# Performance work log

Measured on AMD Instinct MI355X. Metric: run time of the kernel, lower is better.

The kernel has to match this reference:

```python
import jax, jax.numpy as jnp
import numpy as np

EPS = 1e-5
DN = ('NCHW', 'OIHW', 'NCHW')


def ternarize(w):
    """Ternary Weight Network quantization with straight-through estimator.
    delta = 0.7 * mean|w|; alpha = mean of |w| over kept entries.
    """
    aw = jnp.abs(w)
    delta = 0.7 * aw.mean()
    mask = (aw > delta).astype(w.dtype)
    alpha = (aw * mask).sum() / jnp.maximum(mask.sum(), 1.0)
    q = alpha * jnp.sign(w) * mask
    return w + jax.lax.stop_gradient(q - w)


def bn(y, g, b, m, v):
    scale = (g / jnp.sqrt(v + EPS))[None, :, None, None]
    shift = (b - m * g / jnp.sqrt(v + EPS))[None, :, None, None]
    return y * scale + shift


def relu6(y):
    return jnp.clip(y, 0.0, 6.0)


def conv(x, w, stride=1, padding='VALID'):
    return jax.lax.conv_general_dilated(
        x, w, window_strides=(stride, stride), padding=padding,
        dimension_numbers=DN)


def setup_inputs() -> dict:
    key = jax.random.key(0)
    ks = jax.random.split(key, 16)
    inp, oup, expand = 32, 32, 6
    hidden = inp * expand  # 192
    B, H, W = 16, 112, 112
    d = {}
    d['x'] = jax.random.normal(ks[0], (B, inp, H, W), dtype=jnp.float32)
    # 1x1 expand conv
    d['w1'] = jax.random.normal(ks[1], (hidden, inp, 1, 1), dtype=jnp.float32) * 0.1
    d['g1'] = 1.0 + 0.1 * jax.random.normal(ks[2], (hidden,), dtype=jnp.float32)
    d['b1'] = 0.1 * jax.random.normal(ks[3], (hidden,), dtype=jnp.float32)
    d['m1'] = 0.1 * jax.random.normal(ks[4], (hidden,), dtype=jnp.float32)
    d['v1'] = jax.random.uniform(ks[5], (hidden,), minval=0.5, maxval=1.5, dtype=jnp.float32)
    # 3x3 dense conv (no groups in the source -> dense, not depthwise)
    d['w2'] = jax.random.normal(ks[6], (hidden, hidden, 3, 3), dtype=jnp.float32) * 0.05
    d['g2'] = 1.0 + 0.1 * jax.random.normal(ks[7], (hidden,), dtype=jnp.float32)
    d['b2'] = 0.1 * jax.random.normal(ks[8], (hidden,), dtype=jnp.float32)
    d['m2'] = 0.1 * jax.random.normal(ks[9], (hidden,), dtype=jnp.float32)
    d['v2'] = jax.random.uniform(ks[10], (hidden,), minval=0.5, maxval=1.5, dtype=jnp.float32)
    # 1x1 project conv
    d['w3'] = jax.random.normal(ks[11], (oup, hidden, 1, 1), dtype=jnp.float32) * 0.1
    d['g3'] = 1.0 + 0.1 * jax.random.normal(ks[12], (oup,), dtype=jnp.float32)
    d['b3'] = 0.1 * jax.random.normal(ks[13], (oup,), dtype=jnp.float32)
    d['m3'] = 0.1 * jax.random.normal(ks[14], (oup,), dtype=jnp.float32)
    d['v3'] = jax.random.uniform(ks[15], (oup,), minval=0.5, maxval=1.5, dtype=jnp.float32)
    return d


def reference(x, w1, g1, b1, m1, v1, w2, g2, b2, m2, v2, w3, g3, b3, m3, v3):
    # expand: 1x1 ternary conv -> BN -> ReLU6
    h = relu6(bn(conv(x, ternarize(w1)), g1, b1, m1, v1))
    # 3x3 ternary conv (stride=1, padding=1) -> BN -> ReLU6
    h = relu6(bn(conv(h, ternarize(w2), stride=1, padding=((1, 1), (1, 1))), g2, b2, m2, v2))
    # project: 1x1 ternary conv -> BN (no activation)
    h = bn(conv(h, ternarize(w3)), g3, b3, m3, v3)
    # residual connection (stride==1 and inp==oup)
    return x + h
```

## Files before the change

### kernel.cpp

```cpp
#include <hip/hip_runtime.h>


typedef __bf16 bf16x8 __attribute__((ext_vector_type(8)));
typedef __bf16 bf16x4 __attribute__((ext_vector_type(4)));
typedef float  f32x4  __attribute__((ext_vector_type(4)));

#define EPSBN 1e-5f

__device__ __forceinline__ void glds16(const void* g, void* l) {
  __builtin_amdgcn_global_load_lds(
      (const __attribute__((address_space(1))) void*)g,
      (__attribute__((address_space(3))) void*)l, 16, 0, 0);
}

__device__ __forceinline__ __bf16 tern(float w, float delta) {
  float aw = fabsf(w);
  float q = (aw > delta) ? ((w > 0.0f) ? 1.0f : -1.0f) : 0.0f;
  return (__bf16)q;
}


__global__ void stats_pass1(const float* __restrict__ w1, const float* __restrict__ w2,
                            const float* __restrict__ w3, double* __restrict__ pa) {
  __shared__ double red[256];
  int b = blockIdx.x, tid = threadIdx.x;
  int tix = b >> 5, slice = b & 31;
  const float* w = (tix == 0) ? w1 : (tix == 1) ? w2 : w3;
  int len = (tix == 1) ? 331776 : 6144;
  int per = len >> 5;
  int start = slice * per, end = start + per;
  double s = 0.0;
  for (int i = start + tid; i < end; i += 256) s += (double)fabsf(w[i]);
  red[tid] = s; __syncthreads();
  for (int off = 128; off > 0; off >>= 1) {
    if (tid < off) red[tid] += red[tid + off];
    __syncthreads();
  }
  if (tid == 0) pa[b] = red[0];
}

__global__ void stats_pass2(const float* __restrict__ w1, const float* __restrict__ w2,
                            const float* __restrict__ w3, const double* __restrict__ pa,
                            double* __restrict__ ps2, double* __restrict__ pc2) {
  __shared__ double red[256];
  int b = blockIdx.x, tid = threadIdx.x;
  int tix = b >> 5, slice = b & 31;
  const float* w = (tix == 0) ? w1 : (tix == 1) ? w2 : w3;
  int len = (tix == 1) ? 331776 : 6144;
  double tot = 0.0;
  for (int k = 0; k < 32; ++k) tot += pa[tix * 32 + k];
  float delta = 0.7f * (float)(tot / (double)len);
  int per = len >> 5;
  int start = slice * per, end = start + per;
  double s2 = 0.0, c2 = 0.0;
  for (int i = start + tid; i < end; i += 256) {
    float aw = fabsf(w[i]);
    if (aw > delta) { s2 += (double)aw; c2 += 1.0; }
  }
  red[tid] = s2; __syncthreads();
  for (int off = 128; off > 0; off >>= 1) {
    if (tid < off) red[tid] += red[tid + off];
    __syncthreads();
  }
  if (tid == 0) ps2[b] = red[0];
  __syncthreads();
  red[tid] = c2; __syncthreads();
  for (int off = 128; off > 0; off >>= 1) {
    if (tid < off) red[tid] += red[tid + off];
    __syncthreads();
  }
  if (tid == 0) pc2[b] = red[0];
}

__global__ void pack_kernel(
    const float* __restrict__ w1, const float* __restrict__ w2, const float* __restrict__ w3,
    const float* __restrict__ g1, const float* __restrict__ b1, const float* __restrict__ m1, const float* __restrict__ v1,
    const float* __restrict__ g2, const float* __restrict__ b2, const float* __restrict__ m2, const float* __restrict__ v2,
    const float* __restrict__ g3, const float* __restrict__ b3, const float* __restrict__ m3, const float* __restrict__ v3,
    const double* __restrict__ pa, const double* __restrict__ ps2, const double* __restrict__ pc2,
    __bf16* __restrict__ w1p, __bf16* __restrict__ w2p, __bf16* __restrict__ w3p,
    float* __restrict__ sc1, float* __restrict__ sh1,
    float* __restrict__ sc2, float* __restrict__ sh2,
    float* __restrict__ sc3, float* __restrict__ sh3) {
  __shared__ float sst[6];
  int tid = threadIdx.x;
  if (tid < 3) {
    double tot = 0.0, s2 = 0.0, c2 = 0.0;
    for (int k = 0; k < 32; ++k) {
      tot += pa[tid * 32 + k];
      s2  += ps2[tid * 32 + k];
      c2  += pc2[tid * 32 + k];
    }
    int len = (tid == 1) ? 331776 : 6144;
    sst[tid * 2]     = 0.7f * (float)(tot / (double)len);
    sst[tid * 2 + 1] = (float)(s2 / fmax(c2, 1.0));
  }
  __syncthreads();

  int idx = blockIdx.x * 256 + tid;
  if (idx < 331776) {
    float delta2 = sst[2];
    int c = idx / 6144, rem = idx - c * 6144;
    int co = rem >> 5, r5 = rem & 31;
    int cp = r5 >> 3, lo = r5 & 7;
    int tap = c / 6, cb = c - tap * 6;
    int ci = ((cp ^ ((co >> 2) & 3)) << 3) | lo;
    int cifull = cb * 32 + ci;
    w2p[idx] = tern(w2[(co * 192 + cifull) * 9 + tap], delta2);
    return;
  }
  idx -= 331776;
  if (idx < 6144) {
    int co = idx >> 5, c = (idx >> 3) & 3, lo = idx & 7;
    int ci = ((c ^ ((co >> 2) & 3)) << 3) | lo;
    w1p[idx] = tern(w1[co * 32 + ci], sst[0]);
    return;
  }
  idx -= 6144;
  if (idx < 6144) {
    int kc = idx >> 11, rem = idx & 2047;
    int co = rem >> 6, c = (rem >> 3) & 7, lo = rem & 7;
    int ci = ((c ^ (co & 7)) << 3) | lo;
    w3p[idx] = tern(w3[co * 192 + kc * 64 + ci], sst[4]);
    return;
  }
  idx -= 6144;
  if (idx < 192) {
    float rs = rsqrtf(v1[idx] + EPSBN);
    sc1[idx] = g1[idx] * rs * sst[1];
    sh1[idx] = b1[idx] - m1[idx] * g1[idx] * rs;
    return;
  }
  idx -= 192;
  if (idx < 192) {
    float rs = rsqrtf(v2[idx] + EPSBN);
    sc2[idx] = g2[idx] * rs * sst[3];
    sh2[idx] = b2[idx] - m2[idx] * g2[idx] * rs;
    return;
  }
  idx -= 192;
  if (idx < 32) {
    float rs = rsqrtf(v3[idx] + EPSBN);
    sc3[idx] = g3[idx] * rs * sst[5];
    sh3[idx] = b3[idx] - m3[idx] * g3[idx] * rs;
  }
}

__global__ __launch_bounds__(256)
void conv1_kernel(const float* __restrict__ x, const __bf16* __restrict__ w1p,
                  const float* __restrict__ scale1, const float* __restrict__ shift1,
                  __bf16* __restrict__ h1p) {
  __shared__ __align__(16) char smem[57344];
  char* smA = smem;
  char* smB = smem + 7168;
  char* Pb  = smem;
  int tid = threadIdx.x, lane = tid & 63, wave = tid >> 6;
  int h = blockIdx.x, n = blockIdx.y;

  for (int t = wave; t < 12; t += 4)
    glds16((const char*)w1p + t * 1024 + lane * 16, smB + t * 1024);

  const float* xrow = x + (long)n * 401408 + h * 112;
#pragma unroll
  for (int i = 0; i < 4; ++i) {
    int g = i * 256 + tid;
    if (g < 896) {
      int ci0 = (g / 112) * 4, w = g - (g / 112) * 112;
      const float* p = xrow + ci0 * 12544 + w;
      bf16x4 v;
      v[0] = (__bf16)p[0];
      v[1] = (__bf16)p[12544];
      v[2] = (__bf16)p[25088];
      v[3] = (__bf16)p[37632];
      int col = ((ci0 >> 3) ^ ((w >> 2) & 3));
      *(bf16x4*)(smA + w * 64 + (col << 4) + (ci0 & 7) * 2) = v;
    }
  }
  __syncthreads();

  int mrow = lane & 15, quad = lane >> 4;
  int col16 = (quad ^ ((mrow >> 2) & 3)) * 16;
  int c0 = wave * 48;

  bf16x8 aw[3], bv[7];
#pragma unroll
  for (int ic = 0; ic < 3; ++ic)
    aw[ic] = *(const bf16x8*)(smB + (c0 + ic * 16 + mrow) * 64 + col16);
#pragma unroll
  for (int jp = 0; jp < 7; ++jp)
    bv[jp] = *(const bf16x8*)(smA + (jp * 16 + mrow) * 64 + col16);

  asm volatile("s_waitcnt lgkmcnt(0)" ::: "memory");
  __builtin_amdgcn_s_barrier();
  __builtin_amdgcn_sched_barrier(0);

  f32x4 acc[7][3];
#pragma unroll
  for (int jp = 0; jp < 7; ++jp)
#pragma unroll
    for (int ic = 0; ic < 3; ++ic) acc[jp][ic] = (f32x4)0.0f;

#pragma unroll
  for (int jp = 0; jp < 7; ++jp)
#pragma unroll
    for (int ic = 0; ic < 3; ++ic)
      acc[jp][ic] = __builtin_amdgcn_mfma_f32_16x16x32_bf16(aw[ic], bv[jp], acc[jp][ic], 0, 0, 0);

#pragma unroll
  for (int ic = 0; ic < 3; ++ic) {
    int co0 = c0 + ic * 16 + quad * 4;
    float4 sc = *(const float4*)(scale1 + co0);
    float4 sh = *(const float4*)(shift1 + co0);
    int lch = co0 >> 3;
    int boff = (quad & 1) * 8;
#pragma unroll
    for (int jp = 0; jp < 7; ++jp) {
      int w = jp * 16 + mrow;
      bf16x4 o;
      o[0] = (__bf16)fminf(fmaxf(acc[jp][ic][0] * sc.x + sh.x, 0.0f), 6.0f);
      o[1] = (__bf16)fminf(fmaxf(acc[jp][ic][1] * sc.y + sh.y, 0.0f), 6.0f);
      o[2] = (__bf16)fminf(fmaxf(acc[jp][ic][2] * sc.z + sh.z, 0.0f), 6.0f);
      o[3] = (__bf16)fminf(fmaxf(acc[jp][ic][3] * sc.w + sh.w, 0.0f), 6.0f);
      *(bf16x4*)(Pb + w * 512 + ((lch ^ (w & 31)) << 4) + boff) = o;
    }
  }
  asm volatile("s_waitcnt lgkmcnt(0)" ::: "memory");
  __builtin_amdgcn_s_barrier();
  __builtin_amdgcn_sched_barrier(0);

  __bf16* obase = h1p + ((long)(n * 114 + h + 1) * 114 + 1) * 192;
#pragma unroll
  for (int i = 0; i < 11; ++i) {
    int c = i * 256 + tid;
    if (c < 2688) {
      int w = c / 24, lch = c - w * 24;
      float4 v = *(const float4*)(Pb + w * 512 + ((lch ^ (w & 31)) << 4));
      *(float4*)((char*)obase + c * 16) = v;
    }
  }

  float4 z = make_float4(0.f, 0.f, 0.f, 0.f);
  if (tid < 48) {
    int px = (tid < 24) ? 0 : 113;
    int c8 = (tid < 24) ? tid : tid - 24;
    *(float4*)((char*)h1p + ((long)((n * 114 + h + 1) * 114 + px) * 384) + c8 * 16) = z;
  }
  if (h == 0) {
    for (int c = tid; c < 2736; c += 256)
      *(float4*)((char*)h1p + (long)(n * 114) * 114 * 384 + c * 16) = z;
  }
  if (h == 111) {
    for (int c = tid; c < 2736; c += 256)
      *(float4*)((char*)h1p + (long)(n * 114 + 113) * 114 * 384 + c * 16) = z;
  }
}


#define STAGE_W(TAP, CB, B) do {                                              \
  _Pragma("unroll")                                                           \
  for (int it_ = 0; it_ < 3; ++it_) {                                         \
    int t_ = wave + it_ * 4;                                                  \
    glds16(w2b + (long)((TAP) * 6 + (CB)) * 12288 + t_ * 1024 + lane * 16,    \
           smBb + (B) * 12288 + t_ * 1024);                                   \
  }                                                                           \
} while (0)

#define STAGE_A(CB) do {                                                      \
  _Pragma("unroll")                                                           \
  for (int it_ = 0; it_ < 8; ++it_)                                           \
    if (aoff[it_] >= 0)                                                       \
      glds16(h1b + aoff[it_] + (CB) * 64, smAb + (wave + it_ * 4) * 1024);    \
} while (0)

__global__ __launch_bounds__(256, 2)
void conv2_kernel(const __bf16* __restrict__ h1p, const __bf16* __restrict__ w2p,
                  const float* __restrict__ scale2, const float* __restrict__ shift2,
                  const __bf16* __restrict__ w3p,
                  const float* __restrict__ scale3, const float* __restrict__ shift3,
                  const float* __restrict__ x, float* __restrict__ out) {
  __shared__ __align__(16) char smem[78336];
  char* smAb = smem;
  char* smBb = smem + 29184;
  char* Pb   = smem;
  char* w3l  = smem + 43008;
  int tid = threadIdx.x, lane = tid & 63, wave = tid >> 6;
  int bh = blockIdx.x, n = blockIdx.y;
  int h0 = bh * 2;

  int aoff[8];
#pragma unroll
  for (int it = 0; it < 8; ++it) {
    int t = wave + it * 4;
    int s = t * 64 + lane;
    if (s < 1824) {
      int q = s >> 2, c = s & 3;
      int q_log = c ^ ((q >> 2) & 3);
      int prow = q / 114, pcol = q - prow * 114;
      aoff[it] = ((n * 114 + h0 + prow) * 114 + pcol) * 384 + q_log * 16;
    } else {
      aoff[it] = -1;
    }
  }

  int pg = wave >> 1, cg = wave & 1;
  int mrow = lane & 15, quad = lane >> 4;
  int col16 = (quad ^ ((mrow >> 2) & 3)) * 16;
  const char* h1b = (const char*)h1p;
  const char* w2b = (const char*)w2p;

  f32x4 acc[7][6];
#pragma unroll
  for (int jp = 0; jp < 7; ++jp)
#pragma unroll
    for (int ic = 0; ic < 6; ++ic) acc[jp][ic] = (f32x4)0.0f;

  STAGE_A(0);
  STAGE_W(0, 0, 0);
  STAGE_W(1, 0, 1);

  for (int cb = 0; cb < 6; ++cb) {
#pragma unroll
    for (int tap = 0; tap < 9; ++tap) {
      if (tap <= 6) {
        STAGE_W(tap + 2, cb, (tap + 2) & 3);
        asm volatile("s_waitcnt vmcnt(6)" ::: "memory");
      } else if (tap == 7) {
        asm volatile("s_waitcnt vmcnt(3)" ::: "memory");
      } else {
        asm volatile("s_waitcnt vmcnt(0)" ::: "memory");
      }
      __builtin_amdgcn_s_barrier();
      __builtin_amdgcn_sched_barrier(0);

      const char* bbuf = smBb + (tap & 3) * 12288;
      bf16x8 aw[6];
#pragma unroll
      for (int ic = 0; ic < 6; ++ic)
        aw[ic] = *(const bf16x8*)(bbuf + (cg * 96 + ic * 16 + mrow) * 64 + col16);

      int dy = tap / 3, dx = tap - dy * 3;
      int base = (pg + dy) * 114 + dx;
      __builtin_amdgcn_s_setprio(1);
#pragma unroll
      for (int jp = 0; jp < 7; ++jp) {
        int row = base + jp * 16 + mrow;
        bf16x8 av = *(const bf16x8*)(smAb + row * 64 +
                                     ((quad ^ ((row >> 2) & 3)) * 16));
#pragma unroll
        for (int ic = 0; ic < 6; ++ic)
          acc[jp][ic] = __builtin_amdgcn_mfma_f32_16x16x32_bf16(aw[ic], av, acc[jp][ic], 0, 0, 0);
      }
      __builtin_amdgcn_s_setprio(0);
    }

    if (cb < 5) {
      asm volatile("s_waitcnt lgkmcnt(0)" ::: "memory");
      __builtin_amdgcn_sched_barrier(0);
      __builtin_amdgcn_s_barrier();
      STAGE_A(cb + 1);
      STAGE_W(0, cb + 1, 0);
      STAGE_W(1, cb + 1, 1);
    }
  }

  asm volatile("s_waitcnt lgkmcnt(0)" ::: "memory");
  __builtin_amdgcn_s_barrier();
  __builtin_amdgcn_sched_barrier(0);

#pragma unroll
  for (int it = 0; it < 3; ++it) {
    int t = wave + it * 4;
    glds16((const char*)w3p + t * 1024 + lane * 16, w3l + t * 1024);
  }

  int cohalf = wave & 1;
  int co3 = cohalf * 16 + mrow;
  float sc3v = scale3[co3], sh3v = shift3[co3];
  int fbase = (wave >> 1) * 4;

#pragma unroll
  for (int rg = 0; rg < 2; ++rg) {
    if (pg == rg) {
#pragma unroll
      for (int ic = 0; ic < 6; ++ic) {
        int co0 = cg * 96 + ic * 16 + quad * 4;
        float4 sc = *(const float4*)(scale2 + co0);
        float4 sh = *(const float4*)(shift2 + co0);
        int kc = co0 >> 6, c6 = co0 & 63;
        int chunk = c6 >> 3, off = c6 & 7;
#pragma unroll
        for (int jp = 0; jp < 7; ++jp) {
          int px = jp * 16 + mrow;
          bf16x4 o;
          o[0] = (__bf16)fminf(fmaxf(acc[jp][ic][0] * sc.x + sh.x, 0.0f), 6.0f);
          o[1] = (__bf16)fminf(fmaxf(acc[jp][ic][1] * sc.y + sh.y, 0.0f), 6.0f);
          o[2] = (__bf16)fminf(fmaxf(acc[jp][ic][2] * sc.z + sh.z, 0.0f), 6.0f);
          o[3] = (__bf16)fminf(fmaxf(acc[jp][ic][3] * sc.w + sh.w, 0.0f), 6.0f);
          *(bf16x4*)(Pb + px * 384 + kc * 128 + ((chunk ^ (px & 7)) * 16) + off * 2) = o;
        }
      }
    }
    if (rg == 0)
      asm volatile("s_waitcnt vmcnt(0) lgkmcnt(0)" ::: "memory");
    else
      asm volatile("s_waitcnt lgkmcnt(0)" ::: "memory");
    __builtin_amdgcn_s_barrier();
    __builtin_amdgcn_sched_barrier(0);

    f32x4 acc3[4];
#pragma unroll
    for (int f = 0; f < 4; ++f) acc3[f] = (f32x4)0.0f;
    int swz = mrow & 7;
#pragma unroll
    for (int kc = 0; kc < 3; ++kc) {
      bf16x8 b0 = *(const bf16x8*)(w3l + kc * 4096 + (cohalf * 16 + mrow) * 128 +
                                   ((quad ^ swz) * 16));
      bf16x8 b1 = *(const bf16x8*)(w3l + kc * 4096 + (cohalf * 16 + mrow) * 128 +
                                   (((4 + quad) ^ swz) * 16));
#pragma unroll
      for (int f = 0; f < 4; ++f) {
        if (fbase + f < 7) {
          int pr = (fbase + f) * 16 + mrow;
          bf16x8 a0 = *(const bf16x8*)(Pb + pr * 384 + kc * 128 + ((quad ^ swz) * 16));
          bf16x8 a1 = *(const bf16x8*)(Pb + pr * 384 + kc * 128 + (((4 + quad) ^ swz) * 16));
          acc3[f] = __builtin_amdgcn_mfma_f32_16x16x32_bf16(a0, b0, acc3[f], 0, 0, 0);
          acc3[f] = __builtin_amdgcn_mfma_f32_16x16x32_bf16(a1, b1, acc3[f], 0, 0, 0);
        }
      }
    }
    int h = h0 + rg;
    long obase = ((long)(n * 32 + co3) * 112 + h) * 112;
    const float* xb = x + obase;
    float* ob = out + obase;
#pragma unroll
    for (int f = 0; f < 4; ++f) {
      if (fbase + f < 7) {
        int w0 = (fbase + f) * 16 + quad * 4;
        float4 xv = *(const float4*)(xb + w0);
        float4 o;
        o.x = acc3[f][0] * sc3v + sh3v + xv.x;
        o.y = acc3[f][1] * sc3v + sh3v + xv.y;
        o.z = acc3[f][2] * sc3v + sh3v + xv.z;
        o.w = acc3[f][3] * sc3v + sh3v + xv.w;
        *(float4*)(ob + w0) = o;
      }
    }
    if (rg == 0) {
      asm volatile("s_waitcnt lgkmcnt(0)" ::: "memory");
      __builtin_amdgcn_s_barrier();
      __builtin_amdgcn_sched_barrier(0);
    }
  }
}

extern "C" void kernel_launch(void* const* d_in, const int* in_sizes, int n_in,
                              void* d_out, int out_size, void* d_ws, size_t ws_size,
                              hipStream_t stream) {
  const float* x  = (const float*)d_in[0];
  const float* w1 = (const float*)d_in[1];
  const float* g1 = (const float*)d_in[2];
  const float* b1 = (const float*)d_in[3];
  const float* m1 = (const float*)d_in[4];
  const float* v1 = (const float*)d_in[5];
  const float* w2 = (const float*)d_in[6];
  const float* g2 = (const float*)d_in[7];
  const float* b2 = (const float*)d_in[8];
  const float* m2 = (const float*)d_in[9];
  const float* v2 = (const float*)d_in[10];
  const float* w3 = (const float*)d_in[11];
  const float* g3 = (const float*)d_in[12];
  const float* b3 = (const float*)d_in[13];
  const float* m3 = (const float*)d_in[14];
  const float* v3 = (const float*)d_in[15];
  float* out = (float*)d_out;

  char* ws = (char*)d_ws;
  double* pa    = (double*)(ws + 256);
  double* ps2   = (double*)(ws + 1024);
  double* pc2   = (double*)(ws + 1792);
  float* sc1 = (float*)(ws + 2560);
  float* sh1 = (float*)(ws + 3328);
  float* sc2 = (float*)(ws + 4096);
  float* sh2 = (float*)(ws + 4864);
  float* sc3 = (float*)(ws + 5632);
  float* sh3 = (float*)(ws + 5760);
  __bf16* w1p = (__bf16*)(ws + 8192);
  __bf16* w3p = (__bf16*)(ws + 20480);
  __bf16* w2p = (__bf16*)(ws + 32768);
  __bf16* h1p = (__bf16*)(ws + (1 << 20));

  hipLaunchKernelGGL(stats_pass1, dim3(96), dim3(256), 0, stream, w1, w2, w3, pa);
  hipLaunchKernelGGL(stats_pass2, dim3(96), dim3(256), 0, stream, w1, w2, w3, pa, ps2, pc2);
  hipLaunchKernelGGL(pack_kernel, dim3(1346), dim3(256), 0, stream, w1, w2, w3,
                     g1, b1, m1, v1, g2, b2, m2, v2, g3, b3, m3, v3, pa, ps2, pc2,
                     w1p, w2p, w3p, sc1, sh1, sc2, sh2, sc3, sh3);
  hipLaunchKernelGGL(conv1_kernel, dim3(112, 16), dim3(256), 0, stream, x, w1p, sc1, sh1, h1p);
  hipLaunchKernelGGL(conv2_kernel, dim3(56, 16), dim3(256), 0, stream, h1p, w2p, sc2, sh2,
                     w3p, sc3, sh3, x, out);
}
```

Before: 261.4 us.

## Shrink conv2 LDS to double-buffered weights and load w3 straight into registers

```diff
diff --git a/kernel.cpp b/kernel.cpp
--- a/kernel.cpp
+++ b/kernel.cpp
@@ -278,11 +278,10 @@
                   const __bf16* __restrict__ w3p,
                   const float* __restrict__ scale3, const float* __restrict__ shift3,
                   const float* __restrict__ x, float* __restrict__ out) {
-  __shared__ __align__(16) char smem[78336];
+  __shared__ __align__(16) char smem[53760];
   char* smAb = smem;
   char* smBb = smem + 29184;
   char* Pb   = smem;
-  char* w3l  = smem + 43008;
   int tid = threadIdx.x, lane = tid & 63, wave = tid >> 6;
   int bh = blockIdx.x, n = blockIdx.y;
   int h0 = bh * 2;
@@ -316,23 +315,17 @@
 
   STAGE_A(0);
   STAGE_W(0, 0, 0);
-  STAGE_W(1, 0, 1);
 
   for (int cb = 0; cb < 6; ++cb) {
 #pragma unroll
     for (int tap = 0; tap < 9; ++tap) {
-      if (tap <= 6) {
-        STAGE_W(tap + 2, cb, (tap + 2) & 3);
-        asm volatile("s_waitcnt vmcnt(6)" ::: "memory");
-      } else if (tap == 7) {
-        asm volatile("s_waitcnt vmcnt(3)" ::: "memory");
-      } else {
-        asm volatile("s_waitcnt vmcnt(0)" ::: "memory");
-      }
+      asm volatile("s_waitcnt vmcnt(0)" ::: "memory");
       __builtin_amdgcn_s_barrier();
       __builtin_amdgcn_sched_barrier(0);
-
-      const char* bbuf = smBb + (tap & 3) * 12288;
+      if (tap <= 7)
+        STAGE_W(tap + 1, cb, (tap + 1) & 1);
+
+      const char* bbuf = smBb + (tap & 1) * 12288;
       bf16x8 aw[6];
 #pragma unroll
       for (int ic = 0; ic < 6; ++ic)
@@ -354,29 +347,31 @@
     }
 
     if (cb < 5) {
-      asm volatile("s_waitcnt lgkmcnt(0)" ::: "memory");
+      __builtin_amdgcn_s_barrier();
       __builtin_amdgcn_sched_barrier(0);
-      __builtin_amdgcn_s_barrier();
       STAGE_A(cb + 1);
       STAGE_W(0, cb + 1, 0);
-      STAGE_W(1, cb + 1, 1);
     }
   }
 
   asm volatile("s_waitcnt lgkmcnt(0)" ::: "memory");
   __builtin_amdgcn_s_barrier();
   __builtin_amdgcn_sched_barrier(0);
-
-#pragma unroll
-  for (int it = 0; it < 3; ++it) {
-    int t = wave + it * 4;
-    glds16((const char*)w3p + t * 1024 + lane * 16, w3l + t * 1024);
-  }
 
   int cohalf = wave & 1;
   int co3 = cohalf * 16 + mrow;
   float sc3v = scale3[co3], sh3v = shift3[co3];
   int fbase = (wave >> 1) * 4;
+  int swz = mrow & 7;
+
+  bf16x8 wb0[3], wb1[3];
+#pragma unroll
+  for (int kc = 0; kc < 3; ++kc) {
+    wb0[kc] = *(const bf16x8*)((const char*)w3p + kc * 4096 +
+                               (cohalf * 16 + mrow) * 128 + ((quad ^ swz) * 16));
+    wb1[kc] = *(const bf16x8*)((const char*)w3p + kc * 4096 +
+                               (cohalf * 16 + mrow) * 128 + (((4 + quad) ^ swz) * 16));
+  }
 
 #pragma unroll
   for (int rg = 0; rg < 2; ++rg) {
@@ -400,31 +395,23 @@
         }
       }
     }
-    if (rg == 0)
-      asm volatile("s_waitcnt vmcnt(0) lgkmcnt(0)" ::: "memory");
-    else
-      asm volatile("s_waitcnt lgkmcnt(0)" ::: "memory");
+    asm volatile("s_waitcnt lgkmcnt(0)" ::: "memory");
     __builtin_amdgcn_s_barrier();
     __builtin_amdgcn_sched_barrier(0);
 
     f32x4 acc3[4];
 #pragma unroll
     for (int f = 0; f < 4; ++f) acc3[f] = (f32x4)0.0f;
-    int swz = mrow & 7;
 #pragma unroll
     for (int kc = 0; kc < 3; ++kc) {
-      bf16x8 b0 = *(const bf16x8*)(w3l + kc * 4096 + (cohalf * 16 + mrow) * 128 +
-                                   ((quad ^ swz) * 16));
-      bf16x8 b1 = *(const bf16x8*)(w3l + kc * 4096 + (cohalf * 16 + mrow) * 128 +
-                                   (((4 + quad) ^ swz) * 16));
 #pragma unroll
       for (int f = 0; f < 4; ++f) {
         if (fbase + f < 7) {
           int pr = (fbase + f) * 16 + mrow;
           bf16x8 a0 = *(const bf16x8*)(Pb + pr * 384 + kc * 128 + ((quad ^ swz) * 16));
           bf16x8 a1 = *(const bf16x8*)(Pb + pr * 384 + kc * 128 + (((4 + quad) ^ swz) * 16));
-          acc3[f] = __builtin_amdgcn_mfma_f32_16x16x32_bf16(a0, b0, acc3[f], 0, 0, 0);
-          acc3[f] = __builtin_amdgcn_mfma_f32_16x16x32_bf16(a1, b1, acc3[f], 0, 0, 0);
+          acc3[f] = __builtin_amdgcn_mfma_f32_16x16x32_bf16(a0, wb0[kc], acc3[f], 0, 0, 0);
+          acc3[f] = __builtin_amdgcn_mfma_f32_16x16x32_bf16(a1, wb1[kc], acc3[f], 0, 0, 0);
         }
       }
     }
```

Result: no change. 261.1 us (-0.1%).
